# Performance work log

Measured on AMD Instinct MI355X. Metric: run time of the kernel, lower is better.

The kernel has to match this reference:

```python
import jax, jax.numpy as jnp
import numpy as np

QMAX = 127.0

def _quantize_int8(x, axis):
    """Symmetric dynamic int8 quantization along `axis`. Returns (int8 values, fp32 scale)."""
    amax = jnp.max(jnp.abs(x), axis=axis, keepdims=True)
    scale = jnp.maximum(amax, 1e-8) / QMAX
    q = jnp.clip(jnp.round(x / scale), -QMAX, QMAX).astype(jnp.int8)
    return q, scale


def setup_inputs() -> dict:
    key = jax.random.key(0)
    kx, kw, kb = jax.random.split(key, 3)
    tokens, d_in, d_out = 4096, 4096, 16384
    x = jax.random.normal(kx, (tokens, d_in), dtype=jnp.float32)
    weight = jax.random.normal(kw, (d_out, d_in), dtype=jnp.float32) * (1.0 / np.sqrt(d_in))
    bias = jax.random.normal(kb, (d_out,), dtype=jnp.float32)
    return {"x": x, "weight": weight, "bias": bias}


def reference(x, weight, bias):
    # Quantize activations per-row (over in_features), weights per-output-column.
    xq, sx = _quantize_int8(x, axis=-1)            # [T, in] int8, [T, 1] scale
    wq, sw = _quantize_int8(weight.T, axis=0)      # [in, out] int8, [1, out] scale
    acc = jnp.matmul(xq, wq, preferred_element_type=jnp.int32)  # [T, out] int32
    out = acc.astype(jnp.float32) * sx * sw + bias
    return out
```

## Files before the change

### kernel.cpp

```cpp
#include <hip/hip_runtime.h>
#include <stdint.h>

typedef int   i32x4 __attribute__((ext_vector_type(4)));
typedef float f32x4 __attribute__((ext_vector_type(4)));

#define AS1 __attribute__((address_space(1)))
#define AS3 __attribute__((address_space(3)))
#define G2L16(gp, lp) __builtin_amdgcn_global_load_lds((const AS1 void*)(gp), (AS3 void*)(lp), 16, 0, 0)

template<int COLS>
__global__ __launch_bounds__(256)
void quant_rows_k(const float* __restrict__ src, int8_t* __restrict__ q,
                  float* __restrict__ scale)
{
    constexpr int PER = COLS / 256;
    static_assert(PER == 16, "pack assumes 16 elems/thread");
    const int row = blockIdx.x;
    const int t   = threadIdx.x;
    const float* s = src + (size_t)row * COLS + (size_t)t * PER;

    float v[PER];
    #pragma unroll
    for (int i = 0; i < PER; i += 4) {
        f32x4 x4 = *reinterpret_cast<const f32x4*>(s + i);
        v[i+0] = x4[0]; v[i+1] = x4[1]; v[i+2] = x4[2]; v[i+3] = x4[3];
    }
    float amax = 0.0f;
    #pragma unroll
    for (int i = 0; i < PER; ++i) amax = fmaxf(amax, fabsf(v[i]));

    #pragma unroll
    for (int off = 32; off > 0; off >>= 1)
        amax = fmaxf(amax, __shfl_xor(amax, off, 64));

    __shared__ float red[4];
    if ((t & 63) == 0) red[t >> 6] = amax;
    __syncthreads();
    amax = fmaxf(fmaxf(red[0], red[1]), fmaxf(red[2], red[3]));

    const float sc = fmaxf(amax, 1e-8f) / 127.0f;
    if (t == 0) scale[row] = sc;

    union { i32x4 v4; int8_t b[16]; } pk;
    #pragma unroll
    for (int i = 0; i < PER; ++i) {
        float r = rintf(v[i] / sc);
        r = fminf(127.0f, fmaxf(-127.0f, r));
        pk.b[i] = (int8_t)r;
    }
    *reinterpret_cast<i32x4*>(q + (size_t)row * COLS + (size_t)t * PER) = pk.v4;
}

#define BM 256
#define BN 256
#define BKB 128

__device__ __forceinline__ i32x4 mfma_i8(i32x4 a, i32x4 b, i32x4 c) {
    return __builtin_amdgcn_mfma_i32_16x16x64_i8(a, b, c, 0, 0, 0);
}

template<int P, int WAIT>
__device__ __forceinline__ void phase_fn(
    const int8_t* __restrict__ aB, const int8_t* __restrict__ bB,
    int kc0, int kc1,
    i32x4 (&acc)[8][4], i32x4 (&bf)[4][2],
    const int8_t* __restrict__ g0, int8_t* l0,
    const int8_t* __restrict__ g1, int8_t* l1,
    int t16, bool doStage)
{
    i32x4 a00 = *reinterpret_cast<const i32x4*>(aB + (2*P)   * 2048 + kc0);
    i32x4 a01 = *reinterpret_cast<const i32x4*>(aB + (2*P)   * 2048 + kc1);
    i32x4 a10 = *reinterpret_cast<const i32x4*>(aB + (2*P+1) * 2048 + kc0);
    i32x4 a11 = *reinterpret_cast<const i32x4*>(aB + (2*P+1) * 2048 + kc1);
    if (P == 0) {
        #pragma unroll
        for (int ni = 0; ni < 4; ++ni) {
            bf[ni][0] = *reinterpret_cast<const i32x4*>(bB + ni * 2048 + kc0);
            bf[ni][1] = *reinterpret_cast<const i32x4*>(bB + ni * 2048 + kc1);
        }
    }
    if (doStage) {
        G2L16(g0, l0 + t16);
        G2L16(g1, l1 + t16);
    }
    asm volatile("" ::: "memory");
    __builtin_amdgcn_s_barrier();
    asm volatile("s_waitcnt lgkmcnt(0)" ::: "memory");
    __builtin_amdgcn_sched_barrier(0);
    __builtin_amdgcn_s_setprio(1);
    #pragma unroll
    for (int ni = 0; ni < 4; ++ni) {
        acc[2*P  ][ni] = mfma_i8(a00, bf[ni][0], acc[2*P  ][ni]);
        acc[2*P  ][ni] = mfma_i8(a01, bf[ni][1], acc[2*P  ][ni]);
        acc[2*P+1][ni] = mfma_i8(a10, bf[ni][0], acc[2*P+1][ni]);
        acc[2*P+1][ni] = mfma_i8(a11, bf[ni][1], acc[2*P+1][ni]);
    }
    __builtin_amdgcn_s_setprio(0);
    if (WAIT >= 0) {
        if (doStage) {
            if (WAIT == 4) asm volatile("s_waitcnt vmcnt(4)" ::: "memory");
            else           asm volatile("s_waitcnt vmcnt(2)" ::: "memory");
        } else {
            asm volatile("s_waitcnt vmcnt(0)" ::: "memory");
        }
    }
    asm volatile("" ::: "memory");
    __builtin_amdgcn_s_barrier();
    asm volatile("" ::: "memory");
}

__global__ __launch_bounds__(512, 2)
void gemm_i8_k(const int8_t* __restrict__ A,
               const int8_t* __restrict__ B,
               const float*  __restrict__ sx,
               const float*  __restrict__ sw,
               const float*  __restrict__ bias,
               float* __restrict__ C,
               int M, int N, int K)
{
    __shared__ int8_t lA[2][BM * BKB];
    __shared__ int8_t lB[2][BN * BKB];

    const int t    = threadIdx.x;
    const int lane = t & 63;
    const int wid  = t >> 6;
    const int wm   = wid >> 2;
    const int wn   = wid & 3;

    const int nwg = (int)gridDim.x;
    const int bid = (int)blockIdx.x;
    const int swz = ((nwg & 7) == 0) ? ((bid & 7) * (nwg >> 3) + (bid >> 3)) : bid;
    const int nbn = N / BN;
    const int bm  = swz / nbn;
    const int bn  = swz % nbn;

    const int fr  = lane & 15;
    const int c4  = lane >> 4;
    const int sw8 = fr & 7;
    const int kc0 = ((c4    ) ^ sw8) * 16;
    const int kc1 = ((c4 + 4) ^ sw8) * 16;
    const int8_t* aB0 = &lA[0][(wm * 128 + fr) * BKB];
    const int8_t* aB1 = &lA[1][(wm * 128 + fr) * BKB];
    const int8_t* bB0 = &lB[0][(wn * 64  + fr) * BKB];
    const int8_t* bB1 = &lB[1][(wn * 64  + fr) * BKB];

    const int srow = t >> 3;
    const int skc  = ((t & 7) ^ (srow & 7)) * 16;
    const int t16  = t * 16;
    const int8_t* pA = A + (size_t)(bm * BM + srow) * K + skc;
    const int8_t* pB = B + (size_t)(bn * BN + srow) * K + skc;
    const size_t r64  = (size_t)64  * K;
    const size_t r128 = (size_t)128 * K;

    G2L16(pB,              &lB[0][0]     + t16);
    G2L16(pB + r64,        &lB[0][8192]  + t16);
    G2L16(pB + 2*r64,      &lB[0][16384] + t16);
    G2L16(pB + 3*r64,      &lB[0][24576] + t16);
    G2L16(pA,              &lA[0][0]     + t16);
    G2L16(pA + r128,       &lA[0][16384] + t16);
    G2L16(pA + r64,        &lA[0][8192]  + t16);
    G2L16(pA + r128 + r64, &lA[0][24576] + t16);
    asm volatile("s_waitcnt vmcnt(2)" ::: "memory");
    __builtin_amdgcn_s_barrier();
    asm volatile("" ::: "memory");

    i32x4 acc[8][4] = {};
    i32x4 bf[4][2];

    const int NT = K / BKB;
    for (int tt = 0; tt < NT; tt += 2) {
        {
            const size_t ko = (size_t)(tt + 1) * BKB;
            phase_fn<0,-1>(aB0, bB0, kc0, kc1, acc, bf, pB + ko,              &lB[1][0],     pB + ko + r64,        &lB[1][8192],  t16, true);
            phase_fn<1, 4>(aB0, bB0, kc0, kc1, acc, bf, pB + ko + 2*r64,      &lB[1][16384], pB + ko + 3*r64,      &lB[1][24576], t16, true);
            phase_fn<2,-1>(aB0, bB0, kc0, kc1, acc, bf, pA + ko,              &lA[1][0],     pA + ko + r128,       &lA[1][16384], t16, true);
            phase_fn<3, 2>(aB0, bB0, kc0, kc1, acc, bf, pA + ko + r64,        &lA[1][8192],  pA + ko + r128 + r64, &lA[1][24576], t16, true);
        }
        {
            const bool st = (tt + 2) < NT;
            const size_t ko = st ? (size_t)(tt + 2) * BKB : 0;
            phase_fn<0,-1>(aB1, bB1, kc0, kc1, acc, bf, pB + ko,              &lB[0][0],     pB + ko + r64,        &lB[0][8192],  t16, st);
            phase_fn<1, 4>(aB1, bB1, kc0, kc1, acc, bf, pB + ko + 2*r64,      &lB[0][16384], pB + ko + 3*r64,      &lB[0][24576], t16, st);
            phase_fn<2,-1>(aB1, bB1, kc0, kc1, acc, bf, pA + ko,              &lA[0][0],     pA + ko + r128,       &lA[0][16384], t16, st);
            phase_fn<3, 2>(aB1, bB1, kc0, kc1, acc, bf, pA + ko + r64,        &lA[0][8192],  pA + ko + r128 + r64, &lA[0][24576], t16, st);
        }
    }

    const int r0 = bm * BM + wm * 128 + (c4 << 2);
    const int c0 = bn * BN + wn * 64 + fr;
    #pragma unroll
    for (int ni = 0; ni < 4; ++ni) {
        const int c = c0 + ni * 16;
        const float swc = sw[c];
        const float bc  = bias[c];
        #pragma unroll
        for (int mi = 0; mi < 8; ++mi) {
            const int rb = r0 + mi * 16;
            #pragma unroll
            for (int j = 0; j < 4; ++j) {
                const int r = rb + j;
                C[(size_t)r * N + c] = (float)acc[mi][ni][j] * sx[r] * swc + bc;
            }
        }
    }
}

extern "C" void kernel_launch(void* const* d_in, const int* in_sizes, int n_in,
                              void* d_out, int out_size, void* d_ws, size_t ws_size,
                              hipStream_t stream) {
    const float* x    = (const float*)d_in[0];
    const float* w    = (const float*)d_in[1];
    const float* bias = (const float*)d_in[2];
    float* out = (float*)d_out;

    const int dout   = in_sizes[2];
    const int din    = in_sizes[1] / dout;
    const int tokens = in_sizes[0] / din;

    char* ws = (char*)d_ws;
    float*  sx = (float*)ws;
    float*  sw = (float*)(ws + 16384);
    int8_t* xq = (int8_t*)(ws + 16384 + 65536);
    int8_t* wq = xq + (size_t)tokens * din;

    quant_rows_k<4096><<<tokens, 256, 0, stream>>>(x, xq, sx);
    quant_rows_k<4096><<<dout,   256, 0, stream>>>(w, wq, sw);

    const int grid = (tokens / BM) * (dout / BN);
    gemm_i8_k<<<grid, 512, 0, stream>>>(xq, wq, sx, sw, bias, out, tokens, dout, din);
}
```

Before: 422.8 us.

## Restructure int8 GEMM main loop into K-half phases with prefetched LDS fragments

Replaces the four per-row-pair phases with a per-tile function that splits the K=128 tile into two K-halves and four 16-MFMA phases. LDS fragment reads for the next phase are issued before each barrier, and the explicit lgkmcnt(0) wait and sched_barrier are dropped. The last two tiles are peeled so the staging branch becomes a compile-time template flag. The aim is better overlap of LDS reads and global-to-LDS staging with MFMA work, at the cost of higher register pressure and correctness that now depends on the reordered barrier and vmcnt waits.

```diff
diff --git a/kernel.cpp b/kernel.cpp
--- a/kernel.cpp
+++ b/kernel.cpp
@@ -58,55 +58,139 @@
 __device__ __forceinline__ i32x4 mfma_i8(i32x4 a, i32x4 b, i32x4 c) {
     return __builtin_amdgcn_mfma_i32_16x16x64_i8(a, b, c, 0, 0, 0);
 }
-
-template<int P, int WAIT>
-__device__ __forceinline__ void phase_fn(
+__device__ __forceinline__ i32x4 ldsld(const int8_t* p) {
+    return *reinterpret_cast<const i32x4*>(p);
+}
+#define FENCE asm volatile("" ::: "memory")
+#define BAR   do { FENCE; __builtin_amdgcn_s_barrier(); FENCE; } while (0)
+
+template<bool ST>
+__device__ __forceinline__ void tile_fn(
     const int8_t* __restrict__ aB, const int8_t* __restrict__ bB,
-    int kc0, int kc1,
-    i32x4 (&acc)[8][4], i32x4 (&bf)[4][2],
-    const int8_t* __restrict__ g0, int8_t* l0,
-    const int8_t* __restrict__ g1, int8_t* l1,
-    int t16, bool doStage)
+    int kc0, int kc1, i32x4 (&acc)[8][4],
+    const int8_t* __restrict__ gA, const int8_t* __restrict__ gB,
+    int8_t* lAn, int8_t* lBn,
+    size_t r64, size_t r128, int t16)
 {
-    i32x4 a00 = *reinterpret_cast<const i32x4*>(aB + (2*P)   * 2048 + kc0);
-    i32x4 a01 = *reinterpret_cast<const i32x4*>(aB + (2*P)   * 2048 + kc1);
-    i32x4 a10 = *reinterpret_cast<const i32x4*>(aB + (2*P+1) * 2048 + kc0);
-    i32x4 a11 = *reinterpret_cast<const i32x4*>(aB + (2*P+1) * 2048 + kc1);
-    if (P == 0) {
-        #pragma unroll
-        for (int ni = 0; ni < 4; ++ni) {
-            bf[ni][0] = *reinterpret_cast<const i32x4*>(bB + ni * 2048 + kc0);
-            bf[ni][1] = *reinterpret_cast<const i32x4*>(bB + ni * 2048 + kc1);
-        }
-    }
-    if (doStage) {
-        G2L16(g0, l0 + t16);
-        G2L16(g1, l1 + t16);
-    }
-    asm volatile("" ::: "memory");
-    __builtin_amdgcn_s_barrier();
-    asm volatile("s_waitcnt lgkmcnt(0)" ::: "memory");
-    __builtin_amdgcn_sched_barrier(0);
+    i32x4 A00 = ldsld(aB + 0*2048 + kc0);
+    i32x4 A01 = ldsld(aB + 1*2048 + kc0);
+    i32x4 A02 = ldsld(aB + 2*2048 + kc0);
+    i32x4 A03 = ldsld(aB + 3*2048 + kc0);
+    i32x4 B00 = ldsld(bB + 0*2048 + kc0);
+    i32x4 B01 = ldsld(bB + 1*2048 + kc0);
+    i32x4 B02 = ldsld(bB + 2*2048 + kc0);
+    i32x4 B03 = ldsld(bB + 3*2048 + kc0);
+    if (ST) {
+        G2L16(gB,       lBn + t16);
+        G2L16(gB + r64, lBn + 8192 + t16);
+    }
     __builtin_amdgcn_s_setprio(1);
-    #pragma unroll
-    for (int ni = 0; ni < 4; ++ni) {
-        acc[2*P  ][ni] = mfma_i8(a00, bf[ni][0], acc[2*P  ][ni]);
-        acc[2*P  ][ni] = mfma_i8(a01, bf[ni][1], acc[2*P  ][ni]);
-        acc[2*P+1][ni] = mfma_i8(a10, bf[ni][0], acc[2*P+1][ni]);
-        acc[2*P+1][ni] = mfma_i8(a11, bf[ni][1], acc[2*P+1][ni]);
-    }
+    acc[0][0] = mfma_i8(A00, B00, acc[0][0]);
+    acc[1][0] = mfma_i8(A01, B00, acc[1][0]);
+    acc[2][0] = mfma_i8(A02, B00, acc[2][0]);
+    acc[3][0] = mfma_i8(A03, B00, acc[3][0]);
+    acc[0][1] = mfma_i8(A00, B01, acc[0][1]);
+    acc[1][1] = mfma_i8(A01, B01, acc[1][1]);
+    acc[2][1] = mfma_i8(A02, B01, acc[2][1]);
+    acc[3][1] = mfma_i8(A03, B01, acc[3][1]);
+    acc[0][2] = mfma_i8(A00, B02, acc[0][2]);
+    acc[1][2] = mfma_i8(A01, B02, acc[1][2]);
+    acc[2][2] = mfma_i8(A02, B02, acc[2][2]);
+    acc[3][2] = mfma_i8(A03, B02, acc[3][2]);
+    acc[0][3] = mfma_i8(A00, B03, acc[0][3]);
+    acc[1][3] = mfma_i8(A01, B03, acc[1][3]);
+    acc[2][3] = mfma_i8(A02, B03, acc[2][3]);
+    acc[3][3] = mfma_i8(A03, B03, acc[3][3]);
     __builtin_amdgcn_s_setprio(0);
-    if (WAIT >= 0) {
-        if (doStage) {
-            if (WAIT == 4) asm volatile("s_waitcnt vmcnt(4)" ::: "memory");
-            else           asm volatile("s_waitcnt vmcnt(2)" ::: "memory");
-        } else {
-            asm volatile("s_waitcnt vmcnt(0)" ::: "memory");
-        }
-    }
-    asm volatile("" ::: "memory");
-    __builtin_amdgcn_s_barrier();
-    asm volatile("" ::: "memory");
+    if (ST) asm volatile("s_waitcnt vmcnt(2)" ::: "memory");
+    else    asm volatile("s_waitcnt vmcnt(0)" ::: "memory");
+    BAR;
+    i32x4 A10 = ldsld(aB + 4*2048 + kc0);
+    i32x4 A11 = ldsld(aB + 5*2048 + kc0);
+    i32x4 A12 = ldsld(aB + 6*2048 + kc0);
+    i32x4 A13 = ldsld(aB + 7*2048 + kc0);
+    i32x4 A20 = ldsld(aB + 0*2048 + kc1);
+    i32x4 A21 = ldsld(aB + 1*2048 + kc1);
+    i32x4 A22 = ldsld(aB + 2*2048 + kc1);
+    i32x4 A23 = ldsld(aB + 3*2048 + kc1);
+    i32x4 B10 = ldsld(bB + 0*2048 + kc1);
+    i32x4 B11 = ldsld(bB + 1*2048 + kc1);
+    i32x4 B12 = ldsld(bB + 2*2048 + kc1);
+    i32x4 B13 = ldsld(bB + 3*2048 + kc1);
+    if (ST) {
+        G2L16(gB + 2*r64, lBn + 16384 + t16);
+        G2L16(gB + 3*r64, lBn + 24576 + t16);
+    }
+    __builtin_amdgcn_s_setprio(1);
+    acc[4][0] = mfma_i8(A10, B00, acc[4][0]);
+    acc[5][0] = mfma_i8(A11, B00, acc[5][0]);
+    acc[6][0] = mfma_i8(A12, B00, acc[6][0]);
+    acc[7][0] = mfma_i8(A13, B00, acc[7][0]);
+    acc[4][1] = mfma_i8(A10, B01, acc[4][1]);
+    acc[5][1] = mfma_i8(A11, B01, acc[5][1]);
+    acc[6][1] = mfma_i8(A12, B01, acc[6][1]);
+    acc[7][1] = mfma_i8(A13, B01, acc[7][1]);
+    acc[4][2] = mfma_i8(A10, B02, acc[4][2]);
+    acc[5][2] = mfma_i8(A11, B02, acc[5][2]);
+    acc[6][2] = mfma_i8(A12, B02, acc[6][2]);
+    acc[7][2] = mfma_i8(A13, B02, acc[7][2]);
+    acc[4][3] = mfma_i8(A10, B03, acc[4][3]);
+    acc[5][3] = mfma_i8(A11, B03, acc[5][3]);
+    acc[6][3] = mfma_i8(A12, B03, acc[6][3]);
+    acc[7][3] = mfma_i8(A13, B03, acc[7][3]);
+    __builtin_amdgcn_s_setprio(0);
+    BAR;
+    i32x4 A30 = ldsld(aB + 4*2048 + kc1);
+    i32x4 A31 = ldsld(aB + 5*2048 + kc1);
+    i32x4 A32 = ldsld(aB + 6*2048 + kc1);
+    i32x4 A33 = ldsld(aB + 7*2048 + kc1);
+    if (ST) {
+        G2L16(gA,        lAn + t16);
+        G2L16(gA + r128, lAn + 16384 + t16);
+    }
+    __builtin_amdgcn_s_setprio(1);
+    acc[0][0] = mfma_i8(A20, B10, acc[0][0]);
+    acc[1][0] = mfma_i8(A21, B10, acc[1][0]);
+    acc[2][0] = mfma_i8(A22, B10, acc[2][0]);
+    acc[3][0] = mfma_i8(A23, B10, acc[3][0]);
+    acc[0][1] = mfma_i8(A20, B11, acc[0][1]);
+    acc[1][1] = mfma_i8(A21, B11, acc[1][1]);
+    acc[2][1] = mfma_i8(A22, B11, acc[2][1]);
+    acc[3][1] = mfma_i8(A23, B11, acc[3][1]);
+    acc[0][2] = mfma_i8(A20, B12, acc[0][2]);
+    acc[1][2] = mfma_i8(A21, B12, acc[1][2]);
+    acc[2][2] = mfma_i8(A22, B12, acc[2][2]);
+    acc[3][2] = mfma_i8(A23, B12, acc[3][2]);
+    acc[0][3] = mfma_i8(A20, B13, acc[0][3]);
+    acc[1][3] = mfma_i8(A21, B13, acc[1][3]);
+    acc[2][3] = mfma_i8(A22, B13, acc[2][3]);
+    acc[3][3] = mfma_i8(A23, B13, acc[3][3]);
+    __builtin_amdgcn_s_setprio(0);
+    BAR;
+    if (ST) {
+        G2L16(gA + r64,        lAn + 8192 + t16);
+        G2L16(gA + r128 + r64, lAn + 24576 + t16);
+    }
+    __builtin_amdgcn_s_setprio(1);
+    acc[4][0] = mfma_i8(A30, B10, acc[4][0]);
+    acc[5][0] = mfma_i8(A31, B10, acc[5][0]);
+    acc[6][0] = mfma_i8(A32, B10, acc[6][0]);
+    acc[7][0] = mfma_i8(A33, B10, acc[7][0]);
+    acc[4][1] = mfma_i8(A30, B11, acc[4][1]);
+    acc[5][1] = mfma_i8(A31, B11, acc[5][1]);
+    acc[6][1] = mfma_i8(A32, B11, acc[6][1]);
+    acc[7][1] = mfma_i8(A33, B11, acc[7][1]);
+    acc[4][2] = mfma_i8(A30, B12, acc[4][2]);
+    acc[5][2] = mfma_i8(A31, B12, acc[5][2]);
+    acc[6][2] = mfma_i8(A32, B12, acc[6][2]);
+    acc[7][2] = mfma_i8(A33, B12, acc[7][2]);
+    acc[4][3] = mfma_i8(A30, B13, acc[4][3]);
+    acc[5][3] = mfma_i8(A31, B13, acc[5][3]);
+    acc[6][3] = mfma_i8(A32, B13, acc[6][3]);
+    acc[7][3] = mfma_i8(A33, B13, acc[7][3]);
+    __builtin_amdgcn_s_setprio(0);
+    if (ST) asm volatile("s_waitcnt vmcnt(2)" ::: "memory");
+    BAR;
 }
 
 __global__ __launch_bounds__(512, 2)
@@ -161,29 +245,21 @@
     G2L16(pA + r64,        &lA[0][8192]  + t16);
     G2L16(pA + r128 + r64, &lA[0][24576] + t16);
     asm volatile("s_waitcnt vmcnt(2)" ::: "memory");
-    __builtin_amdgcn_s_barrier();
-    asm volatile("" ::: "memory");
+    BAR;
 
     i32x4 acc[8][4] = {};
-    i32x4 bf[4][2];
 
     const int NT = K / BKB;
-    for (int tt = 0; tt < NT; tt += 2) {
-        {
-            const size_t ko = (size_t)(tt + 1) * BKB;
-            phase_fn<0,-1>(aB0, bB0, kc0, kc1, acc, bf, pB + ko,              &lB[1][0],     pB + ko + r64,        &lB[1][8192],  t16, true);
-            phase_fn<1, 4>(aB0, bB0, kc0, kc1, acc, bf, pB + ko + 2*r64,      &lB[1][16384], pB + ko + 3*r64,      &lB[1][24576], t16, true);
-            phase_fn<2,-1>(aB0, bB0, kc0, kc1, acc, bf, pA + ko,              &lA[1][0],     pA + ko + r128,       &lA[1][16384], t16, true);
-            phase_fn<3, 2>(aB0, bB0, kc0, kc1, acc, bf, pA + ko + r64,        &lA[1][8192],  pA + ko + r128 + r64, &lA[1][24576], t16, true);
-        }
-        {
-            const bool st = (tt + 2) < NT;
-            const size_t ko = st ? (size_t)(tt + 2) * BKB : 0;
-            phase_fn<0,-1>(aB1, bB1, kc0, kc1, acc, bf, pB + ko,              &lB[0][0],     pB + ko + r64,        &lB[0][8192],  t16, st);
-            phase_fn<1, 4>(aB1, bB1, kc0, kc1, acc, bf, pB + ko + 2*r64,      &lB[0][16384], pB + ko + 3*r64,      &lB[0][24576], t16, st);
-            phase_fn<2,-1>(aB1, bB1, kc0, kc1, acc, bf, pA + ko,              &lA[0][0],     pA + ko + r128,       &lA[0][16384], t16, st);
-            phase_fn<3, 2>(aB1, bB1, kc0, kc1, acc, bf, pA + ko + r64,        &lA[0][8192],  pA + ko + r128 + r64, &lA[0][24576], t16, st);
-        }
+    for (int tt = 0; tt + 2 < NT; tt += 2) {
+        const size_t ko1 = (size_t)(tt + 1) * BKB;
+        tile_fn<true>(aB0, bB0, kc0, kc1, acc, pA + ko1, pB + ko1, &lA[1][0], &lB[1][0], r64, r128, t16);
+        const size_t ko2 = (size_t)(tt + 2) * BKB;
+        tile_fn<true>(aB1, bB1, kc0, kc1, acc, pA + ko2, pB + ko2, &lA[0][0], &lB[0][0], r64, r128, t16);
+    }
+    {
+        const size_t ko1 = (size_t)(NT - 1) * BKB;
+        tile_fn<true >(aB0, bB0, kc0, kc1, acc, pA + ko1, pB + ko1, &lA[1][0], &lB[1][0], r64, r128, t16);
+        tile_fn<false>(aB1, bB1, kc0, kc1, acc, pA, pB, &lA[0][0], &lB[0][0], r64, r128, t16);
     }
 
     const int r0 = bm * BM + wm * 128 + (c4 << 2);
```

Result: no change. 415.6 us (-1.7%).
